# Kernel tuning notes

Hardware: AMD Instinct MI355X
Metric: run time of the kernel (lower is better)

Reference implementation:

```python
import jax, jax.numpy as jnp
import numpy as np


def _schedule(epoch):
    # Mirrors SPLoss._adjust_N_ratio_q_t (epoch is a static Python int)
    if epoch <= 25:
        return 0.7, 2
    elif epoch <= 75:
        return 0.8, 0
    elif epoch <= 95:
        return 0.9, 0
    else:
        return 1.0, 0


def setup_inputs() -> dict:
    key = jax.random.key(0)
    k1, k2 = jax.random.split(key)
    B, C = 32768, 1000
    output = jax.random.normal(k1, (B, C), dtype=jnp.float32)
    target = jax.random.randint(k2, (B,), 0, C, dtype=jnp.int64)
    return {"output": output, "target": target, "epoch": 10}


def reference(output, target, epoch):
    N_ratio, q_t = _schedule(epoch)
    B = output.shape[0]
    # fused cross-entropy: log-softmax + per-sample gather
    logp = jax.nn.log_softmax(output, axis=-1)            # [B, C]
    ce_loss = -jnp.take_along_axis(logp, target[:, None], axis=1)[:, 0]  # [B]
    # sort-based quantile threshold
    sorted_ce = jnp.sort(ce_loss)                          # ascending
    lambda_t = sorted_ce[int(B * N_ratio)]
    # power reweight v_t = (1 - ce/lambda)^(1/(q_t-1)), zero past threshold, cap at 10
    exponent = 1.0 / (q_t - 1)
    v_t = (1.0 - ce_loss / lambda_t) ** exponent
    v_t = jnp.where(ce_loss >= lambda_t, 0.0, v_t)
    v_t = jnp.where(v_t >= 10.0, 10.0, v_t)
    return (ce_loss * v_t).mean()
```

## Files before the change

### kernel.cpp

```cpp
#include <hip/hip_runtime.h>
#include <math.h>


#define BLOCK 1024
#define WPB   16

__device__ __forceinline__ unsigned f2u(float f) {
    unsigned u = __float_as_uint(f);
    return (u & 0x80000000u) ? ~u : (u | 0x80000000u);
}
__device__ __forceinline__ float u2f(unsigned u) {
    unsigned b = (u & 0x80000000u) ? (u & 0x7FFFFFFFu) : ~u;
    return __uint_as_float(b);
}

__global__ __launch_bounds__(BLOCK) void sploss_kernel(
        const float* __restrict__ x, const int* __restrict__ tgt,
        const int* __restrict__ epoch_p,
        unsigned* __restrict__ ceu, unsigned* __restrict__ counter,
        float* __restrict__ out, int B, int C)
{
    const int tid  = threadIdx.x;
    const int lane = tid & 63;
    const int wave = tid >> 6;

    int row = blockIdx.x * WPB + wave;
    if (row < B) {
        const float* rp = x + (size_t)row * C;
        int t = tgt[row];
        float tv = rp[t];
        float m = -INFINITY, s = 0.0f;
        const float4* p4 = (const float4*)rp;
        int C4 = C >> 2;
        for (int i = lane; i < C4; i += 64) {
            float4 v = p4[i];
            float mx = fmaxf(fmaxf(v.x, v.y), fmaxf(v.z, v.w));
            if (mx > m) { s *= __expf(m - mx); m = mx; }
            s += __expf(v.x - m) + __expf(v.y - m) + __expf(v.z - m) + __expf(v.w - m);
        }
        for (int i = (C4 << 2) + lane; i < C; i += 64) {
            float v = rp[i];
            if (v > m) { s *= __expf(m - v); m = v; }
            s += __expf(v - m);
        }
        for (int off = 32; off > 0; off >>= 1) {
            float mo = __shfl_down(m, off, 64);
            float so = __shfl_down(s, off, 64);
            float nm = fmaxf(m, mo);
            float a = (m  == nm) ? s  : s  * __expf(m  - nm);
            float b = (mo == nm) ? so : so * __expf(mo - nm);
            m = nm; s = a + b;
        }
        if (lane == 0) {
            float cev = (m + __logf(s)) - tv;
            __hip_atomic_store(&ceu[row], f2u(cev),
                               __ATOMIC_RELAXED, __HIP_MEMORY_SCOPE_AGENT);
        }
    }

    __shared__ unsigned s_old;
    __syncthreads();
    if (tid == 0)
        s_old = __hip_atomic_fetch_add(counter, 1u,
                                       __ATOMIC_ACQ_REL, __HIP_MEMORY_SCOPE_AGENT);
    __syncthreads();
    if (s_old != gridDim.x - 1) return;

    int e = epoch_p[0];
    double nr; int qt;
    if (e <= 25)      { nr = 0.7; qt = 2; }
    else if (e <= 75) { nr = 0.8; qt = 0; }
    else if (e <= 95) { nr = 0.9; qt = 0; }
    else              { nr = 1.0; qt = 0; }
    long long kk = (long long)((double)B * nr);
    if (kk > (long long)B - 1) kk = (long long)B - 1;
    const bool inv = (qt != 2);

    unsigned uv[32];
#pragma unroll
    for (int j = 0; j < 32; ++j) {
        int i = tid + j * BLOCK;
        uv[j] = (i < B) ? __hip_atomic_load(&ceu[i], __ATOMIC_RELAXED,
                                            __HIP_MEMORY_SCOPE_AGENT)
                        : 0xFFFFFFFFu;
    }

    __shared__ unsigned lh[256];
    __shared__ unsigned s_prefix, s_k;
    if (tid == 0) { s_prefix = 0u; s_k = (unsigned)kk; }

    for (int p = 0; p < 4; ++p) {
        if (tid < 256) lh[tid] = 0u;
        __syncthreads();
        const int shift = 24 - 8 * p;
        const unsigned hm   = (p == 0) ? 0u : (0xFFFFFFFFu << (shift + 8));
        const unsigned pref = s_prefix;
#pragma unroll
        for (int j = 0; j < 32; ++j) {
            unsigned u = uv[j];
            if ((u & hm) == (pref & hm))
                atomicAdd(&lh[(u >> shift) & 255u], 1u);
        }
        __syncthreads();
        if (wave == 0) {
            unsigned c0 = lh[4 * lane], c1 = lh[4 * lane + 1];
            unsigned c2 = lh[4 * lane + 2], c3 = lh[4 * lane + 3];
            unsigned c4 = c0 + c1 + c2 + c3;
            unsigned incl = c4;
            for (int off = 1; off < 64; off <<= 1) {
                unsigned tt = __shfl_up(incl, off, 64);
                if (lane >= off) incl += tt;
            }
            unsigned excl = incl - c4;
            unsigned kr = s_k;
            unsigned long long bm = __ballot(excl <= kr && kr < excl + c4);
            int L = __ffsll(bm) - 1;
            if (lane == L) {
                unsigned rem = kr - excl;
                int b; unsigned cum;
                if      (rem < c0)           { b = 0; cum = 0; }
                else if (rem < c0 + c1)      { b = 1; cum = c0; }
                else if (rem < c0 + c1 + c2) { b = 2; cum = c0 + c1; }
                else                         { b = 3; cum = c0 + c1 + c2; }
                s_k = rem - cum;
                s_prefix = pref | ((unsigned)(4 * lane + b) << shift);
            }
        }
        __syncthreads();
    }

    const float lam = u2f(s_prefix);
    float part = 0.0f;
#pragma unroll
    for (int j = 0; j < 32; ++j) {
        int i = tid + j * BLOCK;
        if (i >= B) continue;
        float c = u2f(uv[j]);
        float base = 1.0f - c / lam;
        float v = inv ? (1.0f / base) : base;
        if (c >= lam)       v = 0.0f;
        else if (v >= 10.f) v = 10.0f;
        part += c * v;
    }
    for (int off = 32; off > 0; off >>= 1) part += __shfl_down(part, off, 64);
    __shared__ float wsum[WPB];
    if (lane == 0) wsum[wave] = part;
    __syncthreads();
    if (tid == 0) {
        float tot = 0.0f;
        for (int i = 0; i < WPB; ++i) tot += wsum[i];
        out[0] = tot / (float)B;
    }
}

extern "C" void kernel_launch(void* const* d_in, const int* in_sizes, int n_in,
                              void* d_out, int out_size, void* d_ws, size_t ws_size,
                              hipStream_t stream)
{
    const float* x     = (const float*)d_in[0];
    const int*   tgt   = (const int*)d_in[1];
    const int*   epoch = (const int*)d_in[2];
    int B = in_sizes[1];
    int C = in_sizes[0] / B;

    unsigned* ceu     = (unsigned*)d_ws;
    unsigned* counter = ceu + B;

    hipMemsetAsync(counter, 0, sizeof(unsigned), stream);

    int blocks = (B + WPB - 1) / WPB;
    sploss_kernel<<<blocks, BLOCK, 0, stream>>>(x, tgt, epoch, ceu, counter,
                                                (float*)d_out, B, C);
}
```

Measured before the change: 255.3 us.

## Split fused CE and selection into two kernels with register-resident rows

Measured after the change: 227.0 us. 1.12x faster.

```diff
diff --git a/kernel.cpp b/kernel.cpp
--- a/kernel.cpp
+++ b/kernel.cpp
@@ -1,9 +1,6 @@
 #include <hip/hip_runtime.h>
 #include <math.h>
 
-
-#define BLOCK 1024
-#define WPB   16
 
 __device__ __forceinline__ unsigned f2u(float f) {
     unsigned u = __float_as_uint(f);
@@ -14,106 +11,104 @@
     return __uint_as_float(b);
 }
 
-__global__ __launch_bounds__(BLOCK) void sploss_kernel(
+#define CE_WPB 4
+
+__global__ __launch_bounds__(256) void ce_kernel(
         const float* __restrict__ x, const int* __restrict__ tgt,
-        const int* __restrict__ epoch_p,
-        unsigned* __restrict__ ceu, unsigned* __restrict__ counter,
-        float* __restrict__ out, int B, int C)
+        unsigned* __restrict__ ceu, int B, int C)
 {
+    const int lane = threadIdx.x & 63;
+    const int wave = threadIdx.x >> 6;
+    const int row  = blockIdx.x * CE_WPB + wave;
+    if (row >= B) return;
+
+    const float* rp = x + (size_t)row * C;
+    const int C4 = C >> 2;
+    const float4* p4 = (const float4*)rp;
+
+    const float NEG = -INFINITY;
+    float4 v0 = make_float4(NEG, NEG, NEG, NEG), v1 = v0, v2 = v0, v3 = v0;
+    if (lane       < C4) v0 = p4[lane];
+    if (lane +  64 < C4) v1 = p4[lane + 64];
+    if (lane + 128 < C4) v2 = p4[lane + 128];
+    if (lane + 192 < C4) v3 = p4[lane + 192];
+    const float tv = rp[tgt[row]];
+
+    float m = fmaxf(fmaxf(fmaxf(v0.x, v0.y), fmaxf(v0.z, v0.w)),
+                    fmaxf(fmaxf(v1.x, v1.y), fmaxf(v1.z, v1.w)));
+    m = fmaxf(m, fmaxf(fmaxf(v2.x, v2.y), fmaxf(v2.z, v2.w)));
+    m = fmaxf(m, fmaxf(fmaxf(v3.x, v3.y), fmaxf(v3.z, v3.w)));
+    for (int off = 32; off > 0; off >>= 1)
+        m = fmaxf(m, __shfl_xor(m, off, 64));
+
+    float s = __expf(v0.x - m) + __expf(v0.y - m) + __expf(v0.z - m) + __expf(v0.w - m)
+            + __expf(v1.x - m) + __expf(v1.y - m) + __expf(v1.z - m) + __expf(v1.w - m)
+            + __expf(v2.x - m) + __expf(v2.y - m) + __expf(v2.z - m) + __expf(v2.w - m)
+            + __expf(v3.x - m) + __expf(v3.y - m) + __expf(v3.z - m) + __expf(v3.w - m);
+    for (int off = 32; off > 0; off >>= 1)
+        s += __shfl_xor(s, off, 64);
+
+    if (lane == 0)
+        ceu[row] = f2u((m + __logf(s)) - tv);
+}
+
+#define K2_T 1024
+__global__ __launch_bounds__(K2_T) void select_kernel(
+        const unsigned* __restrict__ ceu, const int* __restrict__ epoch_p,
+        float* __restrict__ out, int B)
+{
+    __shared__ unsigned sv[32768];
+    __shared__ unsigned sh[256];
+    __shared__ unsigned s_prefix, s_k;
+    __shared__ float    s_wsum[K2_T / 64];
+
     const int tid  = threadIdx.x;
     const int lane = tid & 63;
     const int wave = tid >> 6;
 
-    int row = blockIdx.x * WPB + wave;
-    if (row < B) {
-        const float* rp = x + (size_t)row * C;
-        int t = tgt[row];
-        float tv = rp[t];
-        float m = -INFINITY, s = 0.0f;
-        const float4* p4 = (const float4*)rp;
-        int C4 = C >> 2;
-        for (int i = lane; i < C4; i += 64) {
-            float4 v = p4[i];
-            float mx = fmaxf(fmaxf(v.x, v.y), fmaxf(v.z, v.w));
-            if (mx > m) { s *= __expf(m - mx); m = mx; }
-            s += __expf(v.x - m) + __expf(v.y - m) + __expf(v.z - m) + __expf(v.w - m);
-        }
-        for (int i = (C4 << 2) + lane; i < C; i += 64) {
-            float v = rp[i];
-            if (v > m) { s *= __expf(m - v); m = v; }
-            s += __expf(v - m);
-        }
-        for (int off = 32; off > 0; off >>= 1) {
-            float mo = __shfl_down(m, off, 64);
-            float so = __shfl_down(s, off, 64);
-            float nm = fmaxf(m, mo);
-            float a = (m  == nm) ? s  : s  * __expf(m  - nm);
-            float b = (mo == nm) ? so : so * __expf(mo - nm);
-            m = nm; s = a + b;
-        }
-        if (lane == 0) {
-            float cev = (m + __logf(s)) - tv;
-            __hip_atomic_store(&ceu[row], f2u(cev),
-                               __ATOMIC_RELAXED, __HIP_MEMORY_SCOPE_AGENT);
-        }
-    }
+    const uint4* c4 = (const uint4*)ceu;
+    const int n4 = B >> 2;
+    for (int i = tid; i < n4; i += K2_T) ((uint4*)sv)[i] = c4[i];
 
-    __shared__ unsigned s_old;
-    __syncthreads();
-    if (tid == 0)
-        s_old = __hip_atomic_fetch_add(counter, 1u,
-                                       __ATOMIC_ACQ_REL, __HIP_MEMORY_SCOPE_AGENT);
-    __syncthreads();
-    if (s_old != gridDim.x - 1) return;
-
-    int e = epoch_p[0];
+    const int e = epoch_p[0];
     double nr; int qt;
     if (e <= 25)      { nr = 0.7; qt = 2; }
     else if (e <= 75) { nr = 0.8; qt = 0; }
     else if (e <= 95) { nr = 0.9; qt = 0; }
     else              { nr = 1.0; qt = 0; }
-    long long kk = (long long)((double)B * nr);
-    if (kk > (long long)B - 1) kk = (long long)B - 1;
     const bool inv = (qt != 2);
-
-    unsigned uv[32];
-#pragma unroll
-    for (int j = 0; j < 32; ++j) {
-        int i = tid + j * BLOCK;
-        uv[j] = (i < B) ? __hip_atomic_load(&ceu[i], __ATOMIC_RELAXED,
-                                            __HIP_MEMORY_SCOPE_AGENT)
-                        : 0xFFFFFFFFu;
+    if (tid == 0) {
+        long long kk = (long long)((double)B * nr);
+        if (kk > (long long)B - 1) kk = (long long)B - 1;
+        s_prefix = 0u;
+        s_k = (unsigned)kk;
     }
-
-    __shared__ unsigned lh[256];
-    __shared__ unsigned s_prefix, s_k;
-    if (tid == 0) { s_prefix = 0u; s_k = (unsigned)kk; }
+    __syncthreads();
 
     for (int p = 0; p < 4; ++p) {
-        if (tid < 256) lh[tid] = 0u;
+        if (tid < 256) sh[tid] = 0u;
         __syncthreads();
         const int shift = 24 - 8 * p;
-        const unsigned hm   = (p == 0) ? 0u : (0xFFFFFFFFu << (shift + 8));
+        const unsigned hm   = p ? (0xFFFFFFFFu << (shift + 8)) : 0u;
         const unsigned pref = s_prefix;
-#pragma unroll
-        for (int j = 0; j < 32; ++j) {
-            unsigned u = uv[j];
+        for (int j = tid; j < B; j += K2_T) {
+            unsigned u = sv[j];
             if ((u & hm) == (pref & hm))
-                atomicAdd(&lh[(u >> shift) & 255u], 1u);
+                atomicAdd(&sh[(u >> shift) & 255u], 1u);
         }
         __syncthreads();
         if (wave == 0) {
-            unsigned c0 = lh[4 * lane], c1 = lh[4 * lane + 1];
-            unsigned c2 = lh[4 * lane + 2], c3 = lh[4 * lane + 3];
-            unsigned c4 = c0 + c1 + c2 + c3;
-            unsigned incl = c4;
+            unsigned c0 = sh[4 * lane], c1 = sh[4 * lane + 1];
+            unsigned c2 = sh[4 * lane + 2], c3 = sh[4 * lane + 3];
+            unsigned cw = c0 + c1 + c2 + c3;
+            unsigned incl = cw;
             for (int off = 1; off < 64; off <<= 1) {
-                unsigned tt = __shfl_up(incl, off, 64);
-                if (lane >= off) incl += tt;
+                unsigned t = __shfl_up(incl, off, 64);
+                if (lane >= off) incl += t;
             }
-            unsigned excl = incl - c4;
+            unsigned excl = incl - cw;
             unsigned kr = s_k;
-            unsigned long long bm = __ballot(excl <= kr && kr < excl + c4);
+            unsigned long long bm = __ballot(excl <= kr && kr < excl + cw);
             int L = __ffsll(bm) - 1;
             if (lane == L) {
                 unsigned rem = kr - excl;
@@ -131,24 +126,20 @@
 
     const float lam = u2f(s_prefix);
     float part = 0.0f;
-#pragma unroll
-    for (int j = 0; j < 32; ++j) {
-        int i = tid + j * BLOCK;
-        if (i >= B) continue;
-        float c = u2f(uv[j]);
+    for (int j = tid; j < B; j += K2_T) {
+        float c = u2f(sv[j]);
         float base = 1.0f - c / lam;
         float v = inv ? (1.0f / base) : base;
         if (c >= lam)       v = 0.0f;
         else if (v >= 10.f) v = 10.0f;
         part += c * v;
     }
-    for (int off = 32; off > 0; off >>= 1) part += __shfl_down(part, off, 64);
-    __shared__ float wsum[WPB];
-    if (lane == 0) wsum[wave] = part;
+    for (int off = 32; off > 0; off >>= 1) part += __shfl_xor(part, off, 64);
+    if (lane == 0) s_wsum[wave] = part;
     __syncthreads();
     if (tid == 0) {
         float tot = 0.0f;
-        for (int i = 0; i < WPB; ++i) tot += wsum[i];
+        for (int i = 0; i < K2_T / 64; ++i) tot += s_wsum[i];
         out[0] = tot / (float)B;
     }
 }
@@ -163,12 +154,9 @@
     int B = in_sizes[1];
     int C = in_sizes[0] / B;
 
-    unsigned* ceu     = (unsigned*)d_ws;
-    unsigned* counter = ceu + B;
+    unsigned* ceu = (unsigned*)d_ws;
 
-    hipMemsetAsync(counter, 0, sizeof(unsigned), stream);
-
-    int blocks = (B + WPB - 1) / WPB;
-    sploss_kernel<<<blocks, BLOCK, 0, stream>>>(x, tgt, epoch, ceu, counter,
-                                                (float*)d_out, B, C);
+    int ceBlocks = (B + CE_WPB - 1) / CE_WPB;
+    ce_kernel<<<ceBlocks, 256, 0, stream>>>(x, tgt, ceu, B, C);
+    select_kernel<<<1, K2_T, 0, stream>>>(ceu, epoch, (float*)d_out, B);
 }
```
